# Kernel optimization log

Measured on AMD Instinct MI355X. Metric: run time of the kernel, lower is better.

The kernel has to match this reference:

```python
import jax, jax.numpy as jnp
import numpy as np

N_WG = 256                 # waveguides per side
N_TOTAL = N_WG * N_WG      # 65536 field points
NNZ = 16 * N_TOTAL         # ~16 couplings per waveguide (Knn-banded)
PROP_DIS = 1.0


def setup_inputs() -> dict:
    key = jax.random.key(0)
    k1, k2, k3, k4, k5 = jax.random.split(key, 5)
    row_idx = jax.random.randint(k1, (NNZ,), 0, N_TOTAL, dtype=jnp.int32)
    col_idx = jax.random.randint(k2, (NNZ,), 0, N_TOTAL, dtype=jnp.int32)
    # small coupling values so the explicit Euler scheme stays stable
    A_vals = jax.random.normal(k3, (NNZ,), dtype=jnp.float32) * 0.01
    Ur0 = jax.random.normal(k4, (N_TOTAL, 1), dtype=jnp.float32)
    Ui0 = jax.random.normal(k5, (N_TOTAL, 1), dtype=jnp.float32)
    return {"A_vals": A_vals, "row_idx": row_idx, "col_idx": col_idx,
            "Ur0": Ur0, "Ui0": Ui0, "Euler_steps": 16}


def reference(A_vals, row_idx, col_idx, Ur0, Ui0, Euler_steps):
    """Euler propagation of a complex field U under sparse coupling A:
       dU/dz = i * A @ U  ->  Ur' = Ur - dz*A@Ui ; Ui' = Ui + dz*A@Ur.
       Matches gen_Euler_with_backward_devs.forward (single device block)."""
    dz = PROP_DIS / Euler_steps

    def spmm(x):  # sparse COO matmul: [n, n] @ [n, 1]
        return jax.ops.segment_sum(A_vals[:, None] * x[col_idx], row_idx,
                                   num_segments=N_TOTAL)

    def step(carry, _):
        Ur, Ui = carry
        Ur1 = Ur - dz * spmm(Ui)
        Ui1 = Ui + dz * spmm(Ur)
        return (Ur1, Ui1), None

    (Ur, Ui), _ = jax.lax.scan(step, (Ur0, Ui0), None, length=Euler_steps)
    return Ur + 1j * Ui
```

## Files before the change

kernel.cpp:

```cpp
#include <hip/hip_runtime.h>

#define N_TOTAL 65536
#define NNZ (16 * N_TOTAL)
#define EULER_STEPS 16
#define SLOTS 48
#define P 256
#define PROWS 256
#define CHUNK 1024
#define NCHUNK 1024
#define SCAP 24

#define TPB 1024
#define NBLK 256
#define CPB (NCHUNK / NBLK)
#define NTHREADS (NBLK * TPB)
#define NTASKS (8 * N_TOTAL)
#define UBUF_F2 (N_TOTAL + 512)


__device__ __forceinline__ void ustore(float2* p, float2 v) {
  unsigned long long d = ((unsigned long long)__float_as_uint(v.y) << 32) |
                         (unsigned long long)__float_as_uint(v.x);
  __hip_atomic_store((unsigned long long*)p, d, __ATOMIC_RELAXED,
                     __HIP_MEMORY_SCOPE_AGENT);
}
__device__ __forceinline__ void st_u32(void* p, unsigned v) {
  __hip_atomic_store((unsigned*)p, v, __ATOMIC_RELAXED,
                     __HIP_MEMORY_SCOPE_AGENT);
}
__device__ __forceinline__ void st_u64(void* p, unsigned long long v) {
  __hip_atomic_store((unsigned long long*)p, v, __ATOMIC_RELAXED,
                     __HIP_MEMORY_SCOPE_AGENT);
}

template <bool HEAVY>
__device__ __forceinline__ void grid_barrier(int* bar, int g) {
  __syncthreads();
  if (threadIdx.x == 0) {
    int* flags = bar;
    int* grp = bar + NBLK * 16;
    int* root = grp + 8 * 16;
    const int b = blockIdx.x;
    int prev = __hip_atomic_fetch_add(&grp[(b & 7) << 4], 1, __ATOMIC_RELAXED,
                                      __HIP_MEMORY_SCOPE_AGENT);
    if (prev == 32 * g - 1) {
      int rprev = __hip_atomic_fetch_add(root, 1, __ATOMIC_RELAXED,
                                         __HIP_MEMORY_SCOPE_AGENT);
      if (rprev == 8 * g - 1) {
        for (int i = 0; i < NBLK; ++i)
          st_u32(&flags[i << 4], (unsigned)g);
      } else {
        while (__hip_atomic_load(&flags[b << 4], __ATOMIC_RELAXED,
                                 __HIP_MEMORY_SCOPE_AGENT) < g)
          __builtin_amdgcn_s_sleep(2);
      }
    } else {
      while (__hip_atomic_load(&flags[b << 4], __ATOMIC_RELAXED,
                               __HIP_MEMORY_SCOPE_AGENT) < g)
        __builtin_amdgcn_s_sleep(2);
    }
    if (HEAVY)
      __builtin_amdgcn_fence(__ATOMIC_ACQUIRE, "agent");
  }
  __syncthreads();
}

template <bool FINAL>
__device__ __forceinline__ void euler_step(const int* __restrict__ cntg,
                                           const unsigned* __restrict__ entries,
                                           const float2* __restrict__ src,
                                           float2* __restrict__ dst,
                                           float* __restrict__ UrOut,
                                           float* __restrict__ UiOut, float dz,
                                           int gtid) {
#pragma unroll
  for (int it = 0; it < NTASKS / NTHREADS; ++it) {
    const int task = gtid + it * NTHREADS;
    const int row = task >> 3;
    const int l = task & 7;
    const int c = cntg[row];
    const unsigned* base = entries + row * SLOTS;
    float sR = 0.0f, sI = 0.0f;
    for (int k = 2 * l; k < c; k += 16) {
      uint2 pr = *(const uint2*)(base + k);
      {
        float a = __uint_as_float(pr.x & 0xFFFF0000u);
        float2 u = src[pr.x & 0xFFFFu];
        sR += a * u.x;
        sI += a * u.y;
      }
      if (k + 1 < c) {
        float a = __uint_as_float(pr.y & 0xFFFF0000u);
        float2 u = src[pr.y & 0xFFFFu];
        sR += a * u.x;
        sI += a * u.y;
      }
    }
    sR += __shfl_xor(sR, 1); sI += __shfl_xor(sI, 1);
    sR += __shfl_xor(sR, 2); sI += __shfl_xor(sI, 2);
    sR += __shfl_xor(sR, 4); sI += __shfl_xor(sI, 4);
    if (l == 0) {
      float2 u = src[row];
      if (FINAL) {
        UrOut[row] = u.x - dz * sI;
        UiOut[row] = u.y + dz * sR;
      } else {
        ustore(&dst[row], make_float2(u.x - dz * sI, u.y + dz * sR));
      }
    }
  }
}

__global__ __launch_bounds__(TPB, 4) void mega_kernel(
    const float* __restrict__ A_vals, const int* __restrict__ row_idx,
    const int* __restrict__ col_idx, const float* __restrict__ Ur0,
    const float* __restrict__ Ui0, int* __restrict__ cntg,
    unsigned* __restrict__ entries, int* __restrict__ hist_t,
    uint2* __restrict__ staged, float2* __restrict__ ustep,
    float* __restrict__ UrOut, float* __restrict__ UiOut, int* bar, float dz) {
  __shared__ unsigned ell[PROWS * SLOTS];
  __shared__ int cnt[PROWS];
  __shared__ int hcnt[NCHUNK];
  const int t = threadIdx.x;
  const int b = blockIdx.x;
  const int gtid = b * TPB + t;

  for (int cidx = 0; cidx < CPB; ++cidx) {
    const int chunk = b * CPB + cidx;
    if (t < P) cnt[t] = 0;
    __syncthreads();
    const int e = chunk * CHUNK + t;
    const int r = row_idx[e];
    const int pp = r >> 8;
    const int pos = atomicAdd(&cnt[pp], 1);
    if (pos < SCAP) {
      unsigned lo = (unsigned)col_idx[e] | ((unsigned)(r & 255) << 16);
      unsigned hi = __float_as_uint(A_vals[e]);
      st_u64(&staged[((size_t)pp * NCHUNK + chunk) * SCAP + pos],
             ((unsigned long long)hi << 32) | lo);
    }
    __syncthreads();
    if (t < P) st_u32(&hist_t[t * NCHUNK + chunk], (unsigned)min(cnt[t], SCAP));
    __syncthreads();
  }
  grid_barrier<true>(bar, 1);

  hcnt[t] = hist_t[b * NCHUNK + t];
  if (t < PROWS) cnt[t] = 0;
  __syncthreads();
  {
    const int c = hcnt[t];
    const uint2* seg = staged + ((size_t)b * NCHUNK + t) * SCAP;
    for (int i = 0; i < c; ++i) {
      uint2 el = seg[i];
      int r = (el.x >> 16) & 255;
      int slot = atomicAdd(&cnt[r], 1);
      if (slot < SLOTS) {
        unsigned bv = el.y;
        unsigned rb = (bv + 0x7FFFu + ((bv >> 16) & 1u)) & 0xFFFF0000u;
        ell[r * SLOTS + slot] = (el.x & 0xFFFFu) | rb;
      }
    }
  }
  __syncthreads();
  const int rowbase = b * PROWS;
  for (int idx = 2 * t; idx < PROWS * SLOTS; idx += 2 * TPB) {
    unsigned long long v = ((unsigned long long)ell[idx + 1] << 32) | ell[idx];
    st_u64(&entries[rowbase * SLOTS + idx], v);
  }
  if (t < PROWS) st_u32(&cntg[rowbase + t], (unsigned)min(cnt[t], SLOTS));
  {
    const int lr = t >> 2, l = t & 3;
    int c = cnt[lr];
    if (c > SLOTS) c = SLOTS;
    float sR = 0.0f, sI = 0.0f;
    for (int s = l; s < c; s += 4) {
      unsigned e = ell[lr * SLOTS + s];
      float a = __uint_as_float(e & 0xFFFF0000u);
      int col = (int)(e & 0xFFFFu);
      sR += a * Ur0[col];
      sI += a * Ui0[col];
    }
    sR += __shfl_xor(sR, 1); sI += __shfl_xor(sI, 1);
    sR += __shfl_xor(sR, 2); sI += __shfl_xor(sI, 2);
    if (l == 0) {
      const int row = rowbase + lr;
      ustore(&ustep[row], make_float2(Ur0[row] - dz * sI, Ui0[row] + dz * sR));
    }
  }
  grid_barrier<true>(bar, 2);

  for (int s = 2; s <= EULER_STEPS - 1; ++s) {
    const float2* src = ustep + (size_t)(s - 2) * UBUF_F2;
    float2* dst = (float2*)(ustep + (size_t)(s - 1) * UBUF_F2);
    euler_step<false>(cntg, entries, src, dst, nullptr, nullptr, dz, gtid);
    grid_barrier<false>(bar, s + 1);
  }
  euler_step<true>(cntg, entries, ustep + (size_t)(EULER_STEPS - 2) * UBUF_F2,
                   nullptr, UrOut, UiOut, dz, gtid);
}

extern "C" void kernel_launch(void* const* d_in, const int* in_sizes, int n_in,
                              void* d_out, int out_size, void* d_ws,
                              size_t ws_size, hipStream_t stream) {
  const float* A_vals  = (const float*)d_in[0];
  const int*   row_idx = (const int*)d_in[1];
  const int*   col_idx = (const int*)d_in[2];
  const float* Ur0     = (const float*)d_in[3];
  const float* Ui0     = (const float*)d_in[4];

  char* ws = (char*)d_ws;
  int*      cntg    = (int*)ws;
  unsigned* entries = (unsigned*)(cntg + N_TOTAL);
  int*      hist_t  = (int*)(entries + (size_t)N_TOTAL * SLOTS);
  uint2*    staged  = (uint2*)(hist_t + P * NCHUNK);
  float2*   ustep   = (float2*)(staged + (size_t)P * NCHUNK * SCAP);
  int*      bar     = (int*)(ustep + (size_t)15 * UBUF_F2);

  float* UrOut = (float*)d_out;
  float* UiOut = UrOut + N_TOTAL;
  const float dz = 1.0f / (float)EULER_STEPS;

  hipMemsetAsync(bar, 0, 4240 * sizeof(int), stream);
  mega_kernel<<<NBLK, TPB, 0, stream>>>(A_vals, row_idx, col_idx, Ur0, Ui0,
                                        cntg, entries, hist_t, staged, ustep,
                                        UrOut, UiOut, bar, dz);
}
```

Baseline: 239.8 us.

## Double persistent grid to 512 blocks and replace tree barrier with flag-array barrier

Raises the persistent grid from 256 to 512 blocks of 1024 threads, with launch bounds raised to 8 blocks per CU, so each thread handles one row-task per Euler step instead of two. The hierarchical atomic-counter barrier is replaced by a centralized one: each block writes an arrival flag and block 0's first wavefront polls all flags, then releases everyone. Only the upper 256 blocks run the ELL build and first step. The aim is more parallelism and lower barrier latency, at the cost of needing all 512 blocks co-resident, higher register pressure, and one wavefront serially scanning every arrival flag.

```diff
diff --git a/kernel.cpp b/kernel.cpp
--- a/kernel.cpp
+++ b/kernel.cpp
@@ -11,7 +11,7 @@
 #define SCAP 24
 
 #define TPB 1024
-#define NBLK 256
+#define NBLK 512
 #define CPB (NCHUNK / NBLK)
 #define NTHREADS (NBLK * TPB)
 #define NTASKS (8 * N_TOTAL)
@@ -32,36 +32,38 @@
   __hip_atomic_store((unsigned long long*)p, v, __ATOMIC_RELAXED,
                      __HIP_MEMORY_SCOPE_AGENT);
 }
+__device__ __forceinline__ int ld_flag(const int* p) {
+  return __hip_atomic_load(p, __ATOMIC_RELAXED, __HIP_MEMORY_SCOPE_AGENT);
+}
 
 template <bool HEAVY>
 __device__ __forceinline__ void grid_barrier(int* bar, int g) {
+  int* arr = bar;
+  int* flags = bar + NBLK * 16;
+  const int b = blockIdx.x;
+  const int t = threadIdx.x;
   __syncthreads();
-  if (threadIdx.x == 0) {
-    int* flags = bar;
-    int* grp = bar + NBLK * 16;
-    int* root = grp + 8 * 16;
-    const int b = blockIdx.x;
-    int prev = __hip_atomic_fetch_add(&grp[(b & 7) << 4], 1, __ATOMIC_RELAXED,
-                                      __HIP_MEMORY_SCOPE_AGENT);
-    if (prev == 32 * g - 1) {
-      int rprev = __hip_atomic_fetch_add(root, 1, __ATOMIC_RELAXED,
-                                         __HIP_MEMORY_SCOPE_AGENT);
-      if (rprev == 8 * g - 1) {
-        for (int i = 0; i < NBLK; ++i)
-          st_u32(&flags[i << 4], (unsigned)g);
-      } else {
-        while (__hip_atomic_load(&flags[b << 4], __ATOMIC_RELAXED,
-                                 __HIP_MEMORY_SCOPE_AGENT) < g)
-          __builtin_amdgcn_s_sleep(2);
-      }
-    } else {
-      while (__hip_atomic_load(&flags[b << 4], __ATOMIC_RELAXED,
-                               __HIP_MEMORY_SCOPE_AGENT) < g)
-        __builtin_amdgcn_s_sleep(2);
-    }
-    if (HEAVY)
-      __builtin_amdgcn_fence(__ATOMIC_ACQUIRE, "agent");
-  }
+  if (b == 0) {
+    if (t < 64) {
+      if (t == 0) st_u32(&arr[0], (unsigned)g);
+      for (;;) {
+        bool ok = true;
+#pragma unroll
+        for (int j = 0; j < NBLK / 64; ++j)
+          ok = ok && (ld_flag(&arr[(t + 64 * j) << 4]) >= g);
+        if (__all(ok)) break;
+        __builtin_amdgcn_s_sleep(1);
+      }
+#pragma unroll
+      for (int j = 0; j < NBLK / 64; ++j)
+        st_u32(&flags[(t + 64 * j) << 4], (unsigned)g);
+    }
+  } else if (t == 0) {
+    st_u32(&arr[b << 4], (unsigned)g);
+    while (ld_flag(&flags[b << 4]) < g) __builtin_amdgcn_s_sleep(1);
+  }
+  if (HEAVY && t == 0)
+    __builtin_amdgcn_fence(__ATOMIC_ACQUIRE, "agent");
   __syncthreads();
 }
 
@@ -73,45 +75,41 @@
                                            float* __restrict__ UrOut,
                                            float* __restrict__ UiOut, float dz,
                                            int gtid) {
-#pragma unroll
-  for (int it = 0; it < NTASKS / NTHREADS; ++it) {
-    const int task = gtid + it * NTHREADS;
-    const int row = task >> 3;
-    const int l = task & 7;
-    const int c = cntg[row];
-    const unsigned* base = entries + row * SLOTS;
-    float sR = 0.0f, sI = 0.0f;
-    for (int k = 2 * l; k < c; k += 16) {
-      uint2 pr = *(const uint2*)(base + k);
-      {
-        float a = __uint_as_float(pr.x & 0xFFFF0000u);
-        float2 u = src[pr.x & 0xFFFFu];
-        sR += a * u.x;
-        sI += a * u.y;
-      }
-      if (k + 1 < c) {
-        float a = __uint_as_float(pr.y & 0xFFFF0000u);
-        float2 u = src[pr.y & 0xFFFFu];
-        sR += a * u.x;
-        sI += a * u.y;
-      }
-    }
-    sR += __shfl_xor(sR, 1); sI += __shfl_xor(sI, 1);
-    sR += __shfl_xor(sR, 2); sI += __shfl_xor(sI, 2);
-    sR += __shfl_xor(sR, 4); sI += __shfl_xor(sI, 4);
-    if (l == 0) {
-      float2 u = src[row];
-      if (FINAL) {
-        UrOut[row] = u.x - dz * sI;
-        UiOut[row] = u.y + dz * sR;
-      } else {
-        ustore(&dst[row], make_float2(u.x - dz * sI, u.y + dz * sR));
-      }
-    }
-  }
-}
-
-__global__ __launch_bounds__(TPB, 4) void mega_kernel(
+  const int row = gtid >> 3;
+  const int l = gtid & 7;
+  const int c = cntg[row];
+  const unsigned* base = entries + row * SLOTS;
+  float sR = 0.0f, sI = 0.0f;
+  for (int k = 2 * l; k < c; k += 16) {
+    uint2 pr = *(const uint2*)(base + k);
+    {
+      float a = __uint_as_float(pr.x & 0xFFFF0000u);
+      float2 u = src[pr.x & 0xFFFFu];
+      sR += a * u.x;
+      sI += a * u.y;
+    }
+    if (k + 1 < c) {
+      float a = __uint_as_float(pr.y & 0xFFFF0000u);
+      float2 u = src[pr.y & 0xFFFFu];
+      sR += a * u.x;
+      sI += a * u.y;
+    }
+  }
+  sR += __shfl_xor(sR, 1); sI += __shfl_xor(sI, 1);
+  sR += __shfl_xor(sR, 2); sI += __shfl_xor(sI, 2);
+  sR += __shfl_xor(sR, 4); sI += __shfl_xor(sI, 4);
+  if (l == 0) {
+    float2 u = src[row];
+    if (FINAL) {
+      UrOut[row] = u.x - dz * sI;
+      UiOut[row] = u.y + dz * sR;
+    } else {
+      ustore(&dst[row], make_float2(u.x - dz * sI, u.y + dz * sR));
+    }
+  }
+}
+
+__global__ __launch_bounds__(TPB, 8) void mega_kernel(
     const float* __restrict__ A_vals, const int* __restrict__ row_idx,
     const int* __restrict__ col_idx, const float* __restrict__ Ur0,
     const float* __restrict__ Ui0, int* __restrict__ cntg,
@@ -145,47 +143,52 @@
   }
   grid_barrier<true>(bar, 1);
 
-  hcnt[t] = hist_t[b * NCHUNK + t];
-  if (t < PROWS) cnt[t] = 0;
-  __syncthreads();
-  {
-    const int c = hcnt[t];
-    const uint2* seg = staged + ((size_t)b * NCHUNK + t) * SCAP;
-    for (int i = 0; i < c; ++i) {
-      uint2 el = seg[i];
-      int r = (el.x >> 16) & 255;
-      int slot = atomicAdd(&cnt[r], 1);
-      if (slot < SLOTS) {
-        unsigned bv = el.y;
-        unsigned rb = (bv + 0x7FFFu + ((bv >> 16) & 1u)) & 0xFFFF0000u;
-        ell[r * SLOTS + slot] = (el.x & 0xFFFFu) | rb;
-      }
-    }
-  }
-  __syncthreads();
-  const int rowbase = b * PROWS;
-  for (int idx = 2 * t; idx < PROWS * SLOTS; idx += 2 * TPB) {
-    unsigned long long v = ((unsigned long long)ell[idx + 1] << 32) | ell[idx];
-    st_u64(&entries[rowbase * SLOTS + idx], v);
-  }
-  if (t < PROWS) st_u32(&cntg[rowbase + t], (unsigned)min(cnt[t], SLOTS));
-  {
-    const int lr = t >> 2, l = t & 3;
-    int c = cnt[lr];
-    if (c > SLOTS) c = SLOTS;
-    float sR = 0.0f, sI = 0.0f;
-    for (int s = l; s < c; s += 4) {
-      unsigned e = ell[lr * SLOTS + s];
-      float a = __uint_as_float(e & 0xFFFF0000u);
-      int col = (int)(e & 0xFFFFu);
-      sR += a * Ur0[col];
-      sI += a * Ui0[col];
-    }
-    sR += __shfl_xor(sR, 1); sI += __shfl_xor(sI, 1);
-    sR += __shfl_xor(sR, 2); sI += __shfl_xor(sI, 2);
-    if (l == 0) {
-      const int row = rowbase + lr;
-      ustore(&ustep[row], make_float2(Ur0[row] - dz * sI, Ui0[row] + dz * sR));
+  if (b >= 256) {
+    const int p = b - 256;
+    hcnt[t] = hist_t[p * NCHUNK + t];
+    if (t < PROWS) cnt[t] = 0;
+    __syncthreads();
+    {
+      const int c = hcnt[t];
+      const uint2* seg = staged + ((size_t)p * NCHUNK + t) * SCAP;
+      for (int i = 0; i < c; ++i) {
+        uint2 el = seg[i];
+        int r = (el.x >> 16) & 255;
+        int slot = atomicAdd(&cnt[r], 1);
+        if (slot < SLOTS) {
+          unsigned bv = el.y;
+          unsigned rb = (bv + 0x7FFFu + ((bv >> 16) & 1u)) & 0xFFFF0000u;
+          ell[r * SLOTS + slot] = (el.x & 0xFFFFu) | rb;
+        }
+      }
+    }
+    __syncthreads();
+    const int rowbase = p * PROWS;
+    for (int idx = 2 * t; idx < PROWS * SLOTS; idx += 2 * TPB) {
+      unsigned long long v =
+          ((unsigned long long)ell[idx + 1] << 32) | ell[idx];
+      st_u64(&entries[rowbase * SLOTS + idx], v);
+    }
+    if (t < PROWS) st_u32(&cntg[rowbase + t], (unsigned)min(cnt[t], SLOTS));
+    {
+      const int lr = t >> 2, l = t & 3;
+      int c = cnt[lr];
+      if (c > SLOTS) c = SLOTS;
+      float sR = 0.0f, sI = 0.0f;
+      for (int s = l; s < c; s += 4) {
+        unsigned e = ell[lr * SLOTS + s];
+        float a = __uint_as_float(e & 0xFFFF0000u);
+        int col = (int)(e & 0xFFFFu);
+        sR += a * Ur0[col];
+        sI += a * Ui0[col];
+      }
+      sR += __shfl_xor(sR, 1); sI += __shfl_xor(sI, 1);
+      sR += __shfl_xor(sR, 2); sI += __shfl_xor(sI, 2);
+      if (l == 0) {
+        const int row = rowbase + lr;
+        ustore(&ustep[row],
+               make_float2(Ur0[row] - dz * sI, Ui0[row] + dz * sR));
+      }
     }
   }
   grid_barrier<true>(bar, 2);
@@ -221,7 +224,7 @@
   float* UiOut = UrOut + N_TOTAL;
   const float dz = 1.0f / (float)EULER_STEPS;
 
-  hipMemsetAsync(bar, 0, 4240 * sizeof(int), stream);
+  hipMemsetAsync(bar, 0, 16384 * sizeof(int), stream);
   mega_kernel<<<NBLK, TPB, 0, stream>>>(A_vals, row_idx, col_idx, Ur0, Ui0,
                                         cntg, entries, hist_t, staged, ustep,
                                         UrOut, UiOut, bar, dz);
```

New measurement: 270.1 us. 1.13x slower.

## Replace tree grid barrier with flat per-block flags and prefetch source field

Applied to the files above, without the earlier changes.

Replaces the hierarchical atomic-counter grid barrier with a flat one. Each block writes its own generation flag, and one wavefront polls all 256 flags in parallel with a wave-wide vote. This removes the serial broadcast loop and the chain of atomic increments. Each Euler step also prefetches a slice of the source field so each XCD-grouped block warms its L2 before the gather. The flat polling puts more load traffic on the flag lines, and the prefetch is a guess about block-to-XCD placement.

```diff
diff --git a/kernel.cpp b/kernel.cpp
--- a/kernel.cpp
+++ b/kernel.cpp
@@ -32,36 +32,29 @@
   __hip_atomic_store((unsigned long long*)p, v, __ATOMIC_RELAXED,
                      __HIP_MEMORY_SCOPE_AGENT);
 }
+__device__ __forceinline__ int ld_flag(const int* p) {
+  return __hip_atomic_load(p, __ATOMIC_RELAXED, __HIP_MEMORY_SCOPE_AGENT);
+}
 
 template <bool HEAVY>
 __device__ __forceinline__ void grid_barrier(int* bar, int g) {
   __syncthreads();
-  if (threadIdx.x == 0) {
-    int* flags = bar;
-    int* grp = bar + NBLK * 16;
-    int* root = grp + 8 * 16;
-    const int b = blockIdx.x;
-    int prev = __hip_atomic_fetch_add(&grp[(b & 7) << 4], 1, __ATOMIC_RELAXED,
-                                      __HIP_MEMORY_SCOPE_AGENT);
-    if (prev == 32 * g - 1) {
-      int rprev = __hip_atomic_fetch_add(root, 1, __ATOMIC_RELAXED,
-                                         __HIP_MEMORY_SCOPE_AGENT);
-      if (rprev == 8 * g - 1) {
-        for (int i = 0; i < NBLK; ++i)
-          st_u32(&flags[i << 4], (unsigned)g);
-      } else {
-        while (__hip_atomic_load(&flags[b << 4], __ATOMIC_RELAXED,
-                                 __HIP_MEMORY_SCOPE_AGENT) < g)
-          __builtin_amdgcn_s_sleep(2);
-      }
-    } else {
-      while (__hip_atomic_load(&flags[b << 4], __ATOMIC_RELAXED,
-                               __HIP_MEMORY_SCOPE_AGENT) < g)
-        __builtin_amdgcn_s_sleep(2);
-    }
-    if (HEAVY)
+  const int t = threadIdx.x;
+  if (t < 64) {
+    int* arr = bar;
+    if (t == 0) st_u32(&arr[blockIdx.x << 4], (unsigned)g);
+    for (;;) {
+      bool ok = true;
+#pragma unroll
+      for (int j = 0; j < NBLK / 64; ++j)
+        ok = ok && (ld_flag(&arr[(t + 64 * j) << 4]) >= g);
+      if (__all(ok)) break;
+      __builtin_amdgcn_s_sleep(2);
+    }
+    if (HEAVY && t == 0)
       __builtin_amdgcn_fence(__ATOMIC_ACQUIRE, "agent");
   }
+  __builtin_amdgcn_sched_barrier(0);
   __syncthreads();
 }
 
@@ -73,6 +66,11 @@
                                            float* __restrict__ UrOut,
                                            float* __restrict__ UiOut, float dz,
                                            int gtid) {
+  {
+    const float4* ps = (const float4*)src;
+    float4 v = ps[((blockIdx.x >> 3) << 10) + threadIdx.x];
+    asm volatile("" ::"v"(v.x), "v"(v.y), "v"(v.z), "v"(v.w));
+  }
 #pragma unroll
   for (int it = 0; it < NTASKS / NTHREADS; ++it) {
     const int task = gtid + it * NTHREADS;
@@ -221,7 +219,7 @@
   float* UiOut = UrOut + N_TOTAL;
   const float dz = 1.0f / (float)EULER_STEPS;
 
-  hipMemsetAsync(bar, 0, 4240 * sizeof(int), stream);
+  hipMemsetAsync(bar, 0, 4096 * sizeof(int), stream);
   mega_kernel<<<NBLK, TPB, 0, stream>>>(A_vals, row_idx, col_idx, Ur0, Ui0,
                                         cntg, entries, hist_t, staged, ustep,
                                         UrOut, UiOut, bar, dz);
```

After: 244.0 us. About the same (+1.8%).
